# Kernel optimization log

Hardware: AMD Instinct MI355X
Metric: run time of the kernel (lower is better)

## Reference

```python
import jax, jax.numpy as jnp
import numpy as np


def _graph_conv_mean(x, src, dst, edge_weight, W_rel, W_root, b, num_nodes):
    # messages: gather source features, optionally scale by edge weight
    msg = x[src]  # [E, D]
    if edge_weight is not None:
        msg = msg * edge_weight[:, None]
    # mean aggregation over incoming edges per destination node
    summed = jax.ops.segment_sum(msg, dst, num_segments=num_nodes)  # [N, D]
    count = jax.ops.segment_sum(jnp.ones((src.shape[0],), x.dtype), dst, num_segments=num_nodes)
    mean = summed / jnp.maximum(count, 1.0)[:, None]
    # out = lin_rel(mean) + lin_root(x) + bias
    return mean @ W_rel + x @ W_root + b


def setup_inputs() -> dict:
    key = jax.random.key(0)
    ks = jax.random.split(key, 8)
    N, E, D, H, C = 100000, 1600000, 128, 32, 5
    x = jax.random.normal(ks[0], (N, D), dtype=jnp.float32)
    edge_index = jax.random.randint(ks[1], (2, E), 0, N, dtype=jnp.int64)
    edge_weight = jax.random.uniform(ks[2], (E,), dtype=jnp.float32)
    W_rel1 = jax.random.normal(ks[3], (D, H), dtype=jnp.float32) / np.sqrt(D)
    W_root1 = jax.random.normal(ks[4], (D, H), dtype=jnp.float32) / np.sqrt(D)
    b1 = jnp.zeros((H,), jnp.float32)
    W_rel2 = jax.random.normal(ks[5], (H, C), dtype=jnp.float32) / np.sqrt(H)
    W_root2 = jax.random.normal(ks[6], (H, C), dtype=jnp.float32) / np.sqrt(H)
    b2 = jnp.zeros((C,), jnp.float32)
    return {"x": x, "edge_index": edge_index, "edge_weight": edge_weight,
            "W_rel1": W_rel1, "W_root1": W_root1, "b1": b1,
            "W_rel2": W_rel2, "W_root2": W_root2, "b2": b2}


def reference(x, edge_index, edge_weight, W_rel1, W_root1, b1, W_rel2, W_root2, b2):
    N = x.shape[0]
    src, dst = edge_index[0], edge_index[1]
    # conv1 with edge_weight
    h = _graph_conv_mean(x, src, dst, edge_weight, W_rel1, W_root1, b1, N)
    h = jax.nn.relu(h)
    # dropout is identity at inference (training=False)
    # conv2 without edge_weight
    out = _graph_conv_mean(h, src, dst, None, W_rel2, W_root2, b2, N)
    return jax.nn.log_softmax(out, axis=1)
```

## Files before the change

kernel.cpp:

```cpp
#include <hip/hip_runtime.h>
#include <math.h>

#define N_NODES 100000
#define E_EDGES 1600000
#define D_IN    128
#define H_MID   32
#define C_OUT   5

#define BSHIFT 8
#define BNODES 256
#define NBKT   391
#define BCAP   4500
#define SRC_BITS 17
#define SRC_MASK 0x1FFFF

#define EB     2048
#define NBA    782
#define NMF    1563

#define KP 136

typedef __attribute__((ext_vector_type(8))) short bf16x8;
typedef __attribute__((ext_vector_type(4))) float f32x4;

__device__ inline unsigned f2bf(float f) {
    unsigned u = __float_as_uint(f);
    return (u + 0x7FFFu + ((u >> 16) & 1u)) >> 16;
}
__device__ inline float bflo(unsigned v) { return __uint_as_float((v & 0xFFFFu) << 16); }
__device__ inline float bfhi(unsigned v) { return __uint_as_float(v & 0xFFFF0000u); }

__global__ void k_prep(const float* __restrict__ Wrel,
                       const float* __restrict__ Wroot,
                       int* __restrict__ bucket_cursor,
                       unsigned short* __restrict__ wt_g) {
    int tid = threadIdx.x;
    bucket_cursor[tid] = 0;
    for (int i = tid; i < 64 * 128; i += 512) {
        int n = i >> 7, k = i & 127;
        float v = (n < H_MID) ? Wrel[k * H_MID + n] : Wroot[k * H_MID + (n - H_MID)];
        wt_g[i] = (unsigned short)f2bf(v);
    }
}

__global__ __launch_bounds__(512) void k_front(
    const int* __restrict__ src,
    const int* __restrict__ dst,
    const float* __restrict__ ew,
    int* __restrict__ bucket_cursor,
    int2* __restrict__ staged,
    const float* __restrict__ x,
    const unsigned short* __restrict__ wt_g,
    const float* __restrict__ b1,
    unsigned short* __restrict__ xrelh,
    float* __restrict__ xroot) {
    __shared__ __align__(16) char smem[26752];
    int tid = threadIdx.x;

    if (blockIdx.x < NBA) {
        int2*  ebuf   = (int2*)smem;
        short* bbuf   = (short*)(smem + 16384);
        int*   cnt0   = (int*)(smem + 20480);
        int*   cnt1   = (int*)(smem + 22044);
        int*   lstart = (int*)(smem + 23608);
        int*   gbase  = (int*)(smem + 25172);
        int*   totp   = (int*)(smem + 26736);
        int eBase = blockIdx.x * EB;
        int half = tid >> 8;
        int* cntH = half ? cnt1 : cnt0;

        if (tid < NBKT) { cnt0[tid] = 0; cnt1[tid] = 0; }
        __syncthreads();

        int b[4], rank[4], packed[4], wbits[4];
        bool valid[4];
        #pragma unroll
        for (int u = 0; u < 4; ++u) {
            int e = eBase + u * 512 + tid;
            valid[u] = (e < E_EDGES);
            b[u] = 0; rank[u] = 0; packed[u] = 0; wbits[u] = 0;
            if (valid[u]) {
                int d = dst[e];
                int s = src[e];
                wbits[u] = __float_as_int(ew[e]);
                b[u] = d >> BSHIFT;
                packed[u] = ((d & (BNODES - 1)) << SRC_BITS) | s;
                rank[u] = atomicAdd(&cntH[b[u]], 1);
            }
        }
        __syncthreads();

        if (tid < 64) {
            int base = tid * 7;
            int loc[7];
            int s = 0;
            #pragma unroll
            for (int k = 0; k < 7; ++k) {
                int idx = base + k;
                int c = (idx < NBKT) ? (cnt0[idx] + cnt1[idx]) : 0;
                loc[k] = s;
                s += c;
            }
            int run = s;
            #pragma unroll
            for (int off = 1; off < 64; off <<= 1) {
                int t = __shfl_up(run, off, 64);
                if (tid >= off) run += t;
            }
            int excl = run - s;
            #pragma unroll
            for (int k = 0; k < 7; ++k) {
                int idx = base + k;
                if (idx < NBKT) lstart[idx] = excl + loc[k];
            }
            if (tid == 63) *totp = run;
        }
        if (tid < NBKT)
            gbase[tid] = atomicAdd(&bucket_cursor[tid], cnt0[tid] + cnt1[tid]);
        __syncthreads();
        int total = *totp;

        #pragma unroll
        for (int u = 0; u < 4; ++u) {
            if (valid[u]) {
                int rg = rank[u] + (half ? cnt0[b[u]] : 0);
                int slot = lstart[b[u]] + rg;
                ebuf[slot] = make_int2(packed[u], wbits[u]);
                bbuf[slot] = (short)b[u];
            }
        }
        __syncthreads();

        for (int t = tid; t < total; t += 512) {
            int2 ev = ebuf[t];
            int bb = bbuf[t];
            int gpos = gbase[bb] + (t - lstart[bb]);
            if (gpos < BCAP)
                staged[(size_t)bb * BCAP + gpos] = ev;
        }
    } else {
        unsigned short* xs = (unsigned short*)smem;
        int nodeBase = (blockIdx.x - NBA) * 64;

        #pragma unroll
        for (int it = 0; it < 8; ++it) {
            int idx = it * 512 + tid;
            int row = idx >> 6, kp = idx & 63;
            int node = nodeBase + row;
            float2 v = make_float2(0.f, 0.f);
            if (node < N_NODES)
                v = *(const float2*)(x + (size_t)node * D_IN + kp * 2);
            unsigned pk = f2bf(v.x) | (f2bf(v.y) << 16);
            *(unsigned*)(xs + row * KP + kp * 2) = pk;
        }
        __syncthreads();

        int lane = tid & 63;
        int wv = tid >> 6;
        int m = lane & 15;
        int quad = lane >> 4;
        int rowBase = (wv & 3) * 16;
        int ntBase = (wv >> 2) * 2;

        f32x4 acc[2];
        acc[0] = (f32x4){0.f, 0.f, 0.f, 0.f};
        acc[1] = (f32x4){0.f, 0.f, 0.f, 0.f};

        #pragma unroll
        for (int kk = 0; kk < 4; ++kk) {
            int k0 = kk * 32 + quad * 8;
            bf16x8 a = *(const bf16x8*)(xs + (rowBase + m) * KP + k0);
            #pragma unroll
            for (int t = 0; t < 2; ++t) {
                bf16x8 bb = *(const bf16x8*)(wt_g + ((ntBase + t) * 16 + m) * 128 + k0);
                acc[t] = __builtin_amdgcn_mfma_f32_16x16x32_bf16(a, bb, acc[t], 0, 0, 0);
            }
        }

        #pragma unroll
        for (int t = 0; t < 2; ++t) {
            #pragma unroll
            for (int r = 0; r < 4; ++r) {
                int node = nodeBase + rowBase + quad * 4 + r;
                int colg = (ntBase + t) * 16 + m;
                if (node < N_NODES) {
                    if (colg < H_MID) {
                        xrelh[(size_t)node * H_MID + colg] =
                            (unsigned short)f2bf(acc[t][r]);
                    } else {
                        int c = colg - H_MID;
                        xroot[(size_t)node * H_MID + c] = acc[t][r] + b1[c];
                    }
                }
            }
        }
    }
}

__global__ __launch_bounds__(1024) void k_bucket1(
    const int* __restrict__ bucket_cursor,
    const int2* __restrict__ staged,
    const unsigned short* __restrict__ xrelh,
    const float* __restrict__ xroot,
    const float* __restrict__ Wrel2,
    const float* __restrict__ Wroot2,
    const float* __restrict__ b2,
    float* __restrict__ h2rel,
    float* __restrict__ h2root,
    int* __restrict__ csr_srcb,
    int* __restrict__ deg_g,
    int* __restrict__ nst_g) {
    __shared__ int2 ecsr[BCAP];
    __shared__ int hist0[BNODES];
    __shared__ int hist1[BNODES];
    __shared__ int nstart[BNODES];
    __shared__ int cur0[BNODES];
    __shared__ int cur1[BNODES];
    int tid = threadIdx.x;
    int b = blockIdx.x;
    int half = tid >> 9;
    int* histH = half ? hist1 : hist0;
    int* curH  = half ? cur1  : cur0;

    int count = bucket_cursor[b];
    if (count > BCAP) count = BCAP;
    const int2* sp = staged + (size_t)b * BCAP;

    if (tid < BNODES) { hist0[tid] = 0; hist1[tid] = 0; }
    __syncthreads();
    for (int i = tid; i < count; i += 1024)
        atomicAdd(&histH[((unsigned)sp[i].x) >> SRC_BITS], 1);
    __syncthreads();

    if (tid < 64) {
        int base = tid * 4;
        int loc[4];
        int s = 0;
        #pragma unroll
        for (int k = 0; k < 4; ++k) {
            loc[k] = s;
            s += hist0[base + k] + hist1[base + k];
        }
        int run = s;
        #pragma unroll
        for (int off = 1; off < 64; off <<= 1) {
            int t = __shfl_up(run, off, 64);
            if (tid >= off) run += t;
        }
        int excl = run - s;
        #pragma unroll
        for (int k = 0; k < 4; ++k)
            nstart[base + k] = excl + loc[k];
    }
    __syncthreads();
    if (tid < BNODES) {
        int h0 = hist0[tid];
        cur0[tid] = nstart[tid];
        cur1[tid] = nstart[tid] + h0;
        int node = b * BNODES + tid;
        if (node < N_NODES) {
            deg_g[node] = h0 + hist1[tid];
            nst_g[node] = nstart[tid];
        }
    }
    __syncthreads();

    for (int i = tid; i < count; i += 1024) {
        int2 ev = sp[i];
        int local = ((unsigned)ev.x) >> SRC_BITS;
        int pos = atomicAdd(&curH[local], 1);
        ecsr[pos] = make_int2(ev.x & SRC_MASK, ev.y);
    }
    __syncthreads();

    int* outb = csr_srcb + (size_t)b * BCAP;
    for (int i = tid; i < count; i += 1024)
        outb[i] = ecsr[i].x;

    int g = tid >> 4;
    int lane = tid & 15;
    for (int nl = g; nl < BNODES; nl += 64) {
        int node = b * BNODES + nl;
        if (node >= N_NODES) continue;
        int dg = hist0[nl] + hist1[nl];
        int i = nstart[nl];
        int end = i + dg;

        float acc0 = 0.f, acc1 = 0.f;
        for (; i + 8 <= end; i += 8) {
            int2 e[8];
            unsigned v[8];
            #pragma unroll
            for (int u = 0; u < 8; ++u) e[u] = ecsr[i + u];
            #pragma unroll
            for (int u = 0; u < 8; ++u)
                v[u] = *(const unsigned*)(xrelh + (size_t)e[u].x * H_MID + lane * 2);
            #pragma unroll
            for (int u = 0; u < 8; ++u) {
                float w = __int_as_float(e[u].y);
                acc0 += bflo(v[u]) * w;
                acc1 += bfhi(v[u]) * w;
            }
        }
        for (; i < end; ++i) {
            int2 e0 = ecsr[i];
            unsigned v0 = *(const unsigned*)(xrelh + (size_t)e0.x * H_MID + lane * 2);
            float w0 = __int_as_float(e0.y);
            acc0 += bflo(v0) * w0;
            acc1 += bfhi(v0) * w0;
        }

        float inv = 1.0f / fmaxf((float)dg, 1.0f);
        float2 rt = *(const float2*)(xroot + (size_t)node * H_MID + lane * 2);
        float h0 = fmaxf(acc0 * inv + rt.x, 0.f);
        float h1 = fmaxf(acc1 * inv + rt.y, 0.f);

        float p[2 * C_OUT];
        #pragma unroll
        for (int j = 0; j < C_OUT; ++j) {
            p[j]         = h0 * Wrel2[(2 * lane) * C_OUT + j]
                         + h1 * Wrel2[(2 * lane + 1) * C_OUT + j];
            p[C_OUT + j] = h0 * Wroot2[(2 * lane) * C_OUT + j]
                         + h1 * Wroot2[(2 * lane + 1) * C_OUT + j];
        }
        #pragma unroll
        for (int mm = 8; mm > 0; mm >>= 1) {
            #pragma unroll
            for (int j = 0; j < 2 * C_OUT; ++j)
                p[j] += __shfl_xor(p[j], mm, 16);
        }
        if (lane == 0) {
            #pragma unroll
            for (int j = 0; j < C_OUT; ++j) {
                h2rel[(size_t)node * C_OUT + j]  = p[j];
                h2root[(size_t)node * C_OUT + j] = p[C_OUT + j] + b2[j];
            }
        }
    }
}

__global__ __launch_bounds__(256) void k_bucket2(
    const int* __restrict__ deg_g,
    const int* __restrict__ nst_g,
    const int* __restrict__ csr_srcb,
    const float* __restrict__ h2rel,
    const float* __restrict__ h2root,
    float* __restrict__ out) {
    int node = blockIdx.x * 32 + (threadIdx.x >> 3);
    int lane = threadIdx.x & 7;
    int dg  = deg_g[node];
    int beg = (node >> BSHIFT) * BCAP + nst_g[node];
    int end = beg + dg;

    float acc = 0.f;
    if (lane < C_OUT) {
        int i = beg;
        int nfull = dg >> 3;
        if (nfull) {
            int s[8];
            #pragma unroll
            for (int u = 0; u < 8; ++u) s[u] = csr_srcb[i + u];
            for (int bb = 1; bb < nfull; ++bb) {
                float v[8];
                #pragma unroll
                for (int u = 0; u < 8; ++u)
                    v[u] = h2rel[(size_t)s[u] * C_OUT + lane];
                int s2[8];
                #pragma unroll
                for (int u = 0; u < 8; ++u) s2[u] = csr_srcb[i + 8 + u];
                #pragma unroll
                for (int u = 0; u < 8; ++u) acc += v[u];
                #pragma unroll
                for (int u = 0; u < 8; ++u) s[u] = s2[u];
                i += 8;
            }
            #pragma unroll
            for (int u = 0; u < 8; ++u)
                acc += h2rel[(size_t)s[u] * C_OUT + lane];
            i += 8;
        }
        for (; i < end; ++i)
            acc += h2rel[(size_t)csr_srcb[i] * C_OUT + lane];
    }
    float inv = 1.0f / fmaxf((float)dg, 1.0f);
    float o = (lane < C_OUT)
                  ? acc * inv + h2root[(size_t)node * C_OUT + lane]
                  : -INFINITY;
    float m = o;
    #pragma unroll
    for (int dd = 4; dd > 0; dd >>= 1) m = fmaxf(m, __shfl_xor(m, dd, 8));
    float e = (lane < C_OUT) ? expf(o - m) : 0.f;
    float ssum = e;
    #pragma unroll
    for (int dd = 4; dd > 0; dd >>= 1) ssum += __shfl_xor(ssum, dd, 8);
    float lse = m + logf(ssum);
    if (lane < C_OUT)
        out[(size_t)node * C_OUT + lane] = o - lse;
}

extern "C" void kernel_launch(void* const* d_in, const int* in_sizes, int n_in,
                              void* d_out, int out_size, void* d_ws, size_t ws_size,
                              hipStream_t stream) {
    const float* x      = (const float*)d_in[0];
    const int*   ei     = (const int*)d_in[1];
    const float* ew     = (const float*)d_in[2];
    const float* Wrel1  = (const float*)d_in[3];
    const float* Wroot1 = (const float*)d_in[4];
    const float* b1     = (const float*)d_in[5];
    const float* Wrel2  = (const float*)d_in[6];
    const float* Wroot2 = (const float*)d_in[7];
    const float* b2     = (const float*)d_in[8];
    float* out = (float*)d_out;

    const int* src = ei;
    const int* dst = ei + E_EDGES;

    char* ws = (char*)d_ws;
    int*   bucket_cursor = (int*)ws;
    unsigned short* wt_g = (unsigned short*)(bucket_cursor + 512);
    int2*  staged        = (int2*)(wt_g + 64 * 128);
    unsigned short* xrelh = (unsigned short*)(staged + (size_t)NBKT * BCAP);
    float* xroot         = (float*)(xrelh + (size_t)N_NODES * H_MID);
    float* h2rel         = xroot + (size_t)N_NODES * H_MID;
    float* h2root        = h2rel + (size_t)N_NODES * C_OUT;
    int*   csr_srcb      = (int*)(h2root + (size_t)N_NODES * C_OUT);
    int*   deg_g         = csr_srcb + (size_t)NBKT * BCAP;
    int*   nst_g         = deg_g + N_NODES;

    k_prep<<<1, 512, 0, stream>>>(Wrel1, Wroot1, bucket_cursor, wt_g);

    k_front<<<NBA + NMF, 512, 0, stream>>>(src, dst, ew, bucket_cursor, staged,
                                           x, wt_g, b1, xrelh, xroot);

    k_bucket1<<<NBKT, 1024, 0, stream>>>(bucket_cursor, staged,
                                         xrelh, xroot, Wrel2, Wroot2, b2,
                                         h2rel, h2root, csr_srcb, deg_g, nst_g);

    k_bucket2<<<N_NODES / 32, 256, 0, stream>>>(deg_g, nst_g, csr_srcb,
                                                h2rel, h2root, out);
}
```

Baseline: 203.1 us.

## Shard bucket cursors four ways and store layer-2 messages as padded bf16

Splits each destination bucket's global atomic cursor and staging region into four shards chosen by block index, which spreads atomic contention across more addresses. Bucket processing now walks the four shard segments. Layer-2 relational features are stored as bf16 in 8-wide padded rows, so each gathered row fits one 16-byte segment and uses half the bytes. This lowers precision of the aggregated messages and adds a per-shard capacity limit (SCAP 1216) that could overflow if edges skew across shards.

```diff
diff --git a/kernel.cpp b/kernel.cpp
--- a/kernel.cpp
+++ b/kernel.cpp
@@ -10,7 +10,9 @@
 #define BSHIFT 8
 #define BNODES 256
 #define NBKT   391
-#define BCAP   4500
+#define NSH    4
+#define SCAP   1216
+#define BCAPC  (NSH * SCAP)
 #define SRC_BITS 17
 #define SRC_MASK 0x1FFFF
 
@@ -29,13 +31,14 @@
 }
 __device__ inline float bflo(unsigned v) { return __uint_as_float((v & 0xFFFFu) << 16); }
 __device__ inline float bfhi(unsigned v) { return __uint_as_float(v & 0xFFFF0000u); }
+__device__ inline float bf2f(unsigned short u) { return __uint_as_float(((unsigned)u) << 16); }
 
 __global__ void k_prep(const float* __restrict__ Wrel,
                        const float* __restrict__ Wroot,
-                       int* __restrict__ bucket_cursor,
+                       int* __restrict__ cursor4,
                        unsigned short* __restrict__ wt_g) {
     int tid = threadIdx.x;
-    bucket_cursor[tid] = 0;
+    for (int i = tid; i < NBKT * NSH; i += 512) cursor4[i] = 0;
     for (int i = tid; i < 64 * 128; i += 512) {
         int n = i >> 7, k = i & 127;
         float v = (n < H_MID) ? Wrel[k * H_MID + n] : Wroot[k * H_MID + (n - H_MID)];
@@ -47,7 +50,7 @@
     const int* __restrict__ src,
     const int* __restrict__ dst,
     const float* __restrict__ ew,
-    int* __restrict__ bucket_cursor,
+    int* __restrict__ cursor4,
     int2* __restrict__ staged,
     const float* __restrict__ x,
     const unsigned short* __restrict__ wt_g,
@@ -66,6 +69,7 @@
         int*   gbase  = (int*)(smem + 25172);
         int*   totp   = (int*)(smem + 26736);
         int eBase = blockIdx.x * EB;
+        int shard = blockIdx.x & (NSH - 1);
         int half = tid >> 8;
         int* cntH = half ? cnt1 : cnt0;
 
@@ -116,7 +120,8 @@
             if (tid == 63) *totp = run;
         }
         if (tid < NBKT)
-            gbase[tid] = atomicAdd(&bucket_cursor[tid], cnt0[tid] + cnt1[tid]);
+            gbase[tid] = atomicAdd(&cursor4[tid * NSH + shard],
+                                   cnt0[tid] + cnt1[tid]);
         __syncthreads();
         int total = *totp;
 
@@ -135,8 +140,8 @@
             int2 ev = ebuf[t];
             int bb = bbuf[t];
             int gpos = gbase[bb] + (t - lstart[bb]);
-            if (gpos < BCAP)
-                staged[(size_t)bb * BCAP + gpos] = ev;
+            if (gpos < SCAP)
+                staged[((size_t)bb * NSH + shard) * SCAP + gpos] = ev;
         }
     } else {
         unsigned short* xs = (unsigned short*)smem;
@@ -198,19 +203,19 @@
 }
 
 __global__ __launch_bounds__(1024) void k_bucket1(
-    const int* __restrict__ bucket_cursor,
+    const int* __restrict__ cursor4,
     const int2* __restrict__ staged,
     const unsigned short* __restrict__ xrelh,
     const float* __restrict__ xroot,
     const float* __restrict__ Wrel2,
     const float* __restrict__ Wroot2,
     const float* __restrict__ b2,
-    float* __restrict__ h2rel,
+    unsigned short* __restrict__ h2rel8,
     float* __restrict__ h2root,
     int* __restrict__ csr_srcb,
     int* __restrict__ deg_g,
     int* __restrict__ nst_g) {
-    __shared__ int2 ecsr[BCAP];
+    __shared__ int2 ecsr[BCAPC];
     __shared__ int hist0[BNODES];
     __shared__ int hist1[BNODES];
     __shared__ int nstart[BNODES];
@@ -222,14 +227,20 @@
     int* histH = half ? hist1 : hist0;
     int* curH  = half ? cur1  : cur0;
 
-    int count = bucket_cursor[b];
-    if (count > BCAP) count = BCAP;
-    const int2* sp = staged + (size_t)b * BCAP;
+    int cs[NSH];
+    #pragma unroll
+    for (int s = 0; s < NSH; ++s) {
+        int c = cursor4[b * NSH + s];
+        cs[s] = (c > SCAP) ? SCAP : c;
+    }
+    const int2* sp = staged + (size_t)b * NSH * SCAP;
 
     if (tid < BNODES) { hist0[tid] = 0; hist1[tid] = 0; }
     __syncthreads();
-    for (int i = tid; i < count; i += 1024)
-        atomicAdd(&histH[((unsigned)sp[i].x) >> SRC_BITS], 1);
+    #pragma unroll
+    for (int s = 0; s < NSH; ++s)
+        for (int i = tid; i < cs[s]; i += 1024)
+            atomicAdd(&histH[((unsigned)sp[s * SCAP + i].x) >> SRC_BITS], 1);
     __syncthreads();
 
     if (tid < 64) {
@@ -265,15 +276,19 @@
     }
     __syncthreads();
 
-    for (int i = tid; i < count; i += 1024) {
-        int2 ev = sp[i];
-        int local = ((unsigned)ev.x) >> SRC_BITS;
-        int pos = atomicAdd(&curH[local], 1);
-        ecsr[pos] = make_int2(ev.x & SRC_MASK, ev.y);
-    }
+    #pragma unroll
+    for (int s = 0; s < NSH; ++s)
+        for (int i = tid; i < cs[s]; i += 1024) {
+            int2 ev = sp[s * SCAP + i];
+            int local = ((unsigned)ev.x) >> SRC_BITS;
+            int pos = atomicAdd(&curH[local], 1);
+            ecsr[pos] = make_int2(ev.x & SRC_MASK, ev.y);
+        }
     __syncthreads();
 
-    int* outb = csr_srcb + (size_t)b * BCAP;
+    int count = cs[0] + cs[1] + cs[2] + cs[3];
+
+    int* outb = csr_srcb + (size_t)b * BCAPC;
     for (int i = tid; i < count; i += 1024)
         outb[i] = ecsr[i].x;
 
@@ -332,7 +347,7 @@
         if (lane == 0) {
             #pragma unroll
             for (int j = 0; j < C_OUT; ++j) {
-                h2rel[(size_t)node * C_OUT + j]  = p[j];
+                h2rel8[(size_t)node * 8 + j] = (unsigned short)f2bf(p[j]);
                 h2root[(size_t)node * C_OUT + j] = p[C_OUT + j] + b2[j];
             }
         }
@@ -343,13 +358,13 @@
     const int* __restrict__ deg_g,
     const int* __restrict__ nst_g,
     const int* __restrict__ csr_srcb,
-    const float* __restrict__ h2rel,
+    const unsigned short* __restrict__ h2rel8,
     const float* __restrict__ h2root,
     float* __restrict__ out) {
     int node = blockIdx.x * 32 + (threadIdx.x >> 3);
     int lane = threadIdx.x & 7;
     int dg  = deg_g[node];
-    int beg = (node >> BSHIFT) * BCAP + nst_g[node];
+    int beg = (node >> BSHIFT) * BCAPC + nst_g[node];
     int end = beg + dg;
 
     float acc = 0.f;
@@ -364,7 +379,7 @@
                 float v[8];
                 #pragma unroll
                 for (int u = 0; u < 8; ++u)
-                    v[u] = h2rel[(size_t)s[u] * C_OUT + lane];
+                    v[u] = bf2f(h2rel8[(size_t)s[u] * 8 + lane]);
                 int s2[8];
                 #pragma unroll
                 for (int u = 0; u < 8; ++u) s2[u] = csr_srcb[i + 8 + u];
@@ -376,11 +391,11 @@
             }
             #pragma unroll
             for (int u = 0; u < 8; ++u)
-                acc += h2rel[(size_t)s[u] * C_OUT + lane];
+                acc += bf2f(h2rel8[(size_t)s[u] * 8 + lane]);
             i += 8;
         }
         for (; i < end; ++i)
-            acc += h2rel[(size_t)csr_srcb[i] * C_OUT + lane];
+            acc += bf2f(h2rel8[(size_t)csr_srcb[i] * 8 + lane]);
     }
     float inv = 1.0f / fmaxf((float)dg, 1.0f);
     float o = (lane < C_OUT)
@@ -416,26 +431,26 @@
     const int* dst = ei + E_EDGES;
 
     char* ws = (char*)d_ws;
-    int*   bucket_cursor = (int*)ws;
-    unsigned short* wt_g = (unsigned short*)(bucket_cursor + 512);
+    int*   cursor4       = (int*)ws;
+    unsigned short* wt_g = (unsigned short*)(cursor4 + 2048);
     int2*  staged        = (int2*)(wt_g + 64 * 128);
-    unsigned short* xrelh = (unsigned short*)(staged + (size_t)NBKT * BCAP);
+    unsigned short* xrelh = (unsigned short*)(staged + (size_t)NBKT * NSH * SCAP);
     float* xroot         = (float*)(xrelh + (size_t)N_NODES * H_MID);
-    float* h2rel         = xroot + (size_t)N_NODES * H_MID;
-    float* h2root        = h2rel + (size_t)N_NODES * C_OUT;
+    unsigned short* h2rel8 = (unsigned short*)(xroot + (size_t)N_NODES * H_MID);
+    float* h2root        = (float*)(h2rel8 + (size_t)N_NODES * 8);
     int*   csr_srcb      = (int*)(h2root + (size_t)N_NODES * C_OUT);
-    int*   deg_g         = csr_srcb + (size_t)NBKT * BCAP;
+    int*   deg_g         = csr_srcb + (size_t)NBKT * BCAPC;
     int*   nst_g         = deg_g + N_NODES;
 
-    k_prep<<<1, 512, 0, stream>>>(Wrel1, Wroot1, bucket_cursor, wt_g);
-
-    k_front<<<NBA + NMF, 512, 0, stream>>>(src, dst, ew, bucket_cursor, staged,
+    k_prep<<<1, 512, 0, stream>>>(Wrel1, Wroot1, cursor4, wt_g);
+
+    k_front<<<NBA + NMF, 512, 0, stream>>>(src, dst, ew, cursor4, staged,
                                            x, wt_g, b1, xrelh, xroot);
 
-    k_bucket1<<<NBKT, 1024, 0, stream>>>(bucket_cursor, staged,
+    k_bucket1<<<NBKT, 1024, 0, stream>>>(cursor4, staged,
                                          xrelh, xroot, Wrel2, Wroot2, b2,
-                                         h2rel, h2root, csr_srcb, deg_g, nst_g);
+                                         h2rel8, h2root, csr_srcb, deg_g, nst_g);
 
     k_bucket2<<<N_NODES / 32, 256, 0, stream>>>(deg_g, nst_g, csr_srcb,
-                                                h2rel, h2root, out);
-}
+                                                h2rel8, h2root, out);
+}
```

Measured after the change: 205.9 us. Within noise of the previous version (+1.4%).
